# Kernel optimization log

Measured on AMD Instinct MI355X. Metric: run time of the kernel, lower is better.

Reference implementation:

```python
import jax, jax.numpy as jnp
import numpy as np

N = 8192
FEAT = 200
SEG = FEAT // 4  # 50
OUT = 300


def setup_inputs() -> dict:
    key = jax.random.key(0)
    ks = jax.random.split(key, 10)
    x = jax.random.normal(ks[0], (N, FEAT), dtype=jnp.float32)
    # row-normalized-ish dense adjacencies so activations stay O(1)
    A_S = jax.random.uniform(ks[1], (N, N), dtype=jnp.float32) / N
    A_F = jax.random.uniform(ks[2], (N, N), dtype=jnp.float32) / N
    gcn_W = jax.random.normal(ks[3], (SEG, SEG), dtype=jnp.float32) / np.sqrt(SEG)
    gcn_b = jnp.zeros((SEG,), dtype=jnp.float32)
    # 12 forget gates: order s1,s2,s3,f1,f2,f3,s1b,s2b,s3b,f1b,f2b,f3b
    gates_W = jax.random.normal(ks[4], (12, 2 * SEG, SEG), dtype=jnp.float32)
    gates_b = jax.random.normal(ks[5], (12, SEG), dtype=jnp.float32)
    proj_W = jax.random.normal(ks[6], (8 * SEG, OUT), dtype=jnp.float32) / np.sqrt(8 * SEG)
    proj_b = jnp.zeros((OUT,), dtype=jnp.float32)
    return {"x": x, "A_S": A_S, "A_F": A_F, "gcn_W": gcn_W, "gcn_b": gcn_b,
            "gates_W": gates_W, "gates_b": gates_b, "proj_W": proj_W, "proj_b": proj_b}


def _lgfm(x, A_S, A_F, gcn_W, gcn_b, gates_W, gates_b, proj_W, proj_b):
    seg = x.shape[1] // 4

    def gcn(h, A):
        # Kipf GraphConvolution: relu(A @ (h @ W) + b); dropout inactive (eval)
        return jax.nn.relu(A @ (h @ gcn_W) + gcn_b)

    def gate(i, h1, h2):
        a = jax.nn.sigmoid(jnp.concatenate([h1, h2], axis=1) @ gates_W[i] + gates_b[i])
        return a * h1

    GS1, GS2, GS3, GF1, GF2, GF3 = 0, 1, 2, 3, 4, 5
    GS1B, GS2B, GS3B, GF1B, GF2B, GF3B = 6, 7, 8, 9, 10, 11

    x1, x2, x3, x4 = x[:, :seg], x[:, seg:2 * seg], x[:, 2 * seg:3 * seg], x[:, 3 * seg:]

    # forward branch (F path then S gating)
    t1_XF1 = x1 + gcn(x1, A_F)
    t1_XS1 = gcn(x1, A_S)
    t1_XF2 = 0.2 * t1_XS1 + 0.8 * gcn(t1_XF1, A_F)
    t2_XF1 = x2 + gcn(x2, A_F)
    t2_XS1 = gcn(x2, A_S)
    t2_XS1 = t2_XS1 + gate(GS1, t1_XS1, t2_XS1)
    t2_XF2 = 0.2 * t2_XS1 + 0.8 * gcn(t2_XF1, A_F)
    t2_XF2 = gate(GF1, t1_XF2, t2_XF2) + t2_XF2
    t3_XF1 = 0.2 * x3 + 0.8 * gcn(x3, A_F)
    t3_XS1 = gcn(x3, A_S)
    t3_XS1 = t3_XS1 + gate(GS2, t2_XS1, t3_XS1)
    t3_XF2 = 0.2 * t3_XS1 + 0.8 * gcn(t3_XF1, A_F)
    t3_XF2 = gate(GF2, t2_XF2, t3_XF2) + t3_XF2
    t4_XF1 = x4 + gcn(x4, A_F)
    t4_XS1 = gcn(x4, A_S)
    t4_XS1 = t4_XS1 + gate(GS3, t3_XS1, t4_XS1)
    t4_XF2 = 0.2 * t4_XS1 + 0.8 * gcn(t4_XF1, A_F)
    t4_XF2 = gate(GF3, t3_XF2, t4_XF2) + t4_XF2

    # mirrored branch (S path then F gating)
    t1_XS1b = x1 + gcn(x1, A_S)
    t1_XF1b = gcn(x1, A_F)
    t1_XS2 = 0.2 * t1_XF1b + 0.8 * gcn(t1_XS1b, A_S)
    t2_XS1b = x2 + gcn(x2, A_S)
    t2_XF1b = gcn(x2, A_F)
    t2_XF1b = t2_XF1b + gate(GF1B, t1_XF1b, t2_XF1b)
    t2_XS2 = 0.2 * t2_XF1b + 0.8 * gcn(t2_XS1b, A_S)
    t2_XS2 = gate(GS1B, t1_XS2, t2_XS2) + t2_XS2
    t3_XS1b = 0.2 * x3 + 0.8 * gcn(x3, A_S)
    t3_XF1b = gcn(x3, A_F)
    t3_XF1b = t3_XF1b + gate(GF2B, t2_XF1b, t3_XF1b)
    t3_XS2 = 0.2 * t3_XF1b + 0.8 * gcn(t3_XS1b, A_S)
    t3_XS2 = gate(GS2B, t2_XS2, t3_XS2) + t3_XS2
    t4_XS1b = x4 + gcn(x4, A_S)
    t4_XF1b = gcn(x4, A_F)
    t4_XF1b = t4_XF1b + gate(GF3B, t3_XF1b, t4_XF1b)
    t4_XS2 = 0.2 * t4_XF1b + 0.8 * gcn(t4_XS1b, A_S)
    t4_XS2 = gate(GS3B, t3_XS2, t4_XS2) + t4_XS2

    h_L = jnp.concatenate([t1_XF2, t1_XS2, t2_XF2, t2_XS2,
                           t3_XF2, t3_XS2, t4_XF2, t4_XS2], axis=1)
    return h_L @ proj_W + proj_b


def reference(x, A_S, A_F, gcn_W, gcn_b, gates_W, gates_b, proj_W, proj_b):
    return _lgfm(x, A_S, A_F, gcn_W, gcn_b, gates_W, gates_b, proj_W, proj_b)
```

## Files before the change

kernel.cpp:

```cpp
#include <hip/hip_runtime.h>
#include <math.h>

typedef float float4v __attribute__((ext_vector_type(4)));
typedef __attribute__((ext_vector_type(4))) float f32x4;
typedef __attribute__((ext_vector_type(8))) short short8v;
typedef __attribute__((ext_vector_type(8))) unsigned short ushort8v;

#define NROW 8192
#define FEAT 200
#define OUTC 300
#define ZLD  256
#define HLK  448
#define HLN  384

__device__ __forceinline__ unsigned short f2bf(float x) {
  unsigned u = __float_as_uint(x);
  return (unsigned short)((u + 0x7fffu + ((u >> 16) & 1u)) >> 16);
}

__global__ __launch_bounds__(256) void zmul_t_kernel(
    const float* __restrict__ x, const float* __restrict__ W,
    unsigned short* __restrict__ Zt) {
  __shared__ float Ws[2500];
  __shared__ float hs[16][200];
  __shared__ float zbuf[16][256];
  int t = threadIdx.x;
  int r0 = blockIdx.x * 16;
  for (int i = t; i < 2500; i += 256) Ws[i] = W[i];
  for (int i = t; i < 16 * FEAT; i += 256)
    hs[0][i] = x[(size_t)r0 * FEAT + i];
  __syncthreads();
  for (int i = t; i < 16 * 256; i += 256) {
    int row = i >> 8, j = i & 255;
    float acc = 0.f;
    if (j < FEAT) {
      int s = j / 50, jj = j % 50;
      const float* hrow = &hs[row][s * 50];
      #pragma unroll 5
      for (int k = 0; k < 50; ++k) acc += hrow[k] * Ws[k * 50 + jj];
    }
    zbuf[row][j] = acc;
  }
  __syncthreads();
  unsigned int* Ztu = (unsigned int*)Zt;
  for (int i = t; i < 256 * 8; i += 256) {
    int j = i >> 3, w2 = i & 7;
    unsigned int lo = f2bf(zbuf[2 * w2][j]);
    unsigned int hi = f2bf(zbuf[2 * w2 + 1][j]);
    Ztu[((j * NROW + r0) >> 1) + w2] = lo | (hi << 16);
  }
}

__global__ __launch_bounds__(512, 4) void gemm_cvt_spill_kernel(
    const float* __restrict__ AF, const float* __restrict__ AS,
    const unsigned short* __restrict__ ZtF,
    const unsigned short* __restrict__ ZtS,
    float* __restrict__ Cpart,
    unsigned short* __restrict__ AbF_o, unsigned short* __restrict__ AbS_o) {
  int d = blockIdx.x;
  int L = (d & 7) * 64 + (d >> 3);
  int cb  = L & 1;
  int mat = (L >> 1) & 1;
  int ks  = (L >> 2) & 1;
  int rb  = L >> 3;

  const float* __restrict__ A = mat ? AS : AF;
  const unsigned short* __restrict__ Zt = mat ? ZtS : ZtF;
  unsigned short* __restrict__ Abo = mat ? AbS_o : AbF_o;

  int t = threadIdx.x;
  int lane = t & 63, wv = t >> 6;
  int row0 = rb * 128, n0 = cb * 128, k0 = ks * 4096;

  __shared__ short As[2][128 * 64];
  __shared__ short Bs[2][128 * 64];

  int srcAf[2], dstA[2];
  #pragma unroll
  for (int i = 0; i < 2; ++i) {
    int cc = i * 512 + t;
    int m = cc >> 3, s = cc & 7;
    srcAf[i] = (row0 + m) * NROW + s * 8;
    dstA[i] = m * 64 + ((s ^ (m & 7)) * 8);
  }
  int srcB[2], ldsDstB[2];
  #pragma unroll
  for (int i = 0; i < 2; ++i) {
    int c = i * 512 + t;
    int m = c >> 3, sl = c & 7;
    srcB[i] = (n0 + m) * NROW + ((sl ^ (m & 7)) * 8);
    ldsDstB[i] = (i * 512 + wv * 64) * 8;
  }

  f32x4 aA0[2], aA1[2], aB0[2], aB1[2];

#define STAGE_B(buf, kt)                                                              \
  {                                                                                   \
    _Pragma("unroll")                                                                 \
    for (int i = 0; i < 2; ++i)                                                       \
      __builtin_amdgcn_global_load_lds(                                               \
          (const __attribute__((address_space(1))) void*)(Zt + srcB[i] + (kt)),       \
          (__attribute__((address_space(3))) void*)(&Bs[buf][ldsDstB[i]]), 16, 0, 0); \
  }
#define LOAD_BANK(b0, b1, kt)                              \
  {                                                        \
    _Pragma("unroll")                                      \
    for (int i = 0; i < 2; ++i) {                          \
      b0[i] = *(const f32x4*)&A[srcAf[i] + (kt)];          \
      b1[i] = *(const f32x4*)&A[srcAf[i] + (kt) + 4];      \
    }                                                      \
  }
#define WRITE_BANK(buf, b0, b1, kt, spill)                                              \
  {                                                                                     \
    _Pragma("unroll")                                                                   \
    for (int i = 0; i < 2; ++i) {                                                       \
      unsigned u0_, u1_, u2_, u3_;                                                      \
      asm("v_cvt_pk_bf16_f32 %0, %1, %2" : "=v"(u0_) : "v"(b0[i][0]), "v"(b0[i][1]));   \
      asm("v_cvt_pk_bf16_f32 %0, %1, %2" : "=v"(u1_) : "v"(b0[i][2]), "v"(b0[i][3]));   \
      asm("v_cvt_pk_bf16_f32 %0, %1, %2" : "=v"(u2_) : "v"(b1[i][0]), "v"(b1[i][1]));   \
      asm("v_cvt_pk_bf16_f32 %0, %1, %2" : "=v"(u3_) : "v"(b1[i][2]), "v"(b1[i][3]));   \
      union { unsigned u[4]; short8v v; } pk_;                                          \
      pk_.u[0] = u0_; pk_.u[1] = u1_; pk_.u[2] = u2_; pk_.u[3] = u3_;                   \
      *(short8v*)&As[buf][dstA[i]] = pk_.v;                                             \
      if (spill) *(short8v*)&Abo[(size_t)srcAf[i] + (kt)] = pk_.v;                      \
    }                                                                                   \
  }
#define MFMA_TILE(buf)                                                                  \
  {                                                                                     \
    _Pragma("unroll")                                                                   \
    for (int kk = 0; kk < 2; ++kk) {                                                    \
      int slot = kk * 4 + l4;                                                           \
      short8v a[2], b[4];                                                               \
      _Pragma("unroll")                                                                 \
      for (int i = 0; i < 2; ++i) {                                                     \
        int m = m0 + i * 16 + l15;                                                      \
        a[i] = *(const short8v*)&As[buf][m * 64 + ((slot ^ (m & 7)) * 8)];              \
      }                                                                                 \
      _Pragma("unroll")                                                                 \
      for (int j = 0; j < 4; ++j) {                                                     \
        int n = n0w + j * 16 + l15;                                                     \
        b[j] = *(const short8v*)&Bs[buf][n * 64 + ((slot ^ (n & 7)) * 8)];              \
      }                                                                                 \
      _Pragma("unroll")                                                                 \
      for (int i = 0; i < 2; ++i)                                                       \
        _Pragma("unroll")                                                               \
        for (int j = 0; j < 4; ++j)                                                     \
          acc[i][j] = __builtin_amdgcn_mfma_f32_16x16x32_bf16(a[i], b[j], acc[i][j], 0, 0, 0); \
  } }

  f32x4 acc[2][4];
  #pragma unroll
  for (int i = 0; i < 2; ++i)
    #pragma unroll
    for (int j = 0; j < 4; ++j) acc[i][j] = (f32x4)0.f;

  int m0 = (wv >> 1) * 32, n0w = (wv & 1) * 64;
  int l15 = lane & 15, l4 = lane >> 4;

  LOAD_BANK(aA0, aA1, k0)
  LOAD_BANK(aB0, aB1, k0 + 64)
  STAGE_B(0, k0)
  WRITE_BANK(0, aA0, aA1, k0, (cb == 0))
  __syncthreads();

  for (int itp = 0; itp < 32; ++itp) {
    {
      int it = 2 * itp;
      if (it + 1 < 64) STAGE_B(1, k0 + (it + 1) * 64)
      if (it + 2 < 64) LOAD_BANK(aA0, aA1, k0 + (it + 2) * 64)
      MFMA_TILE(0)
      if (it + 1 < 64) {
        bool sp = (cb == ((it + 1) >= 32 ? 1 : 0));
        WRITE_BANK(1, aB0, aB1, k0 + (it + 1) * 64, sp)
      }
      __syncthreads();
    }
    {
      int it = 2 * itp + 1;
      if (it + 1 < 64) STAGE_B(0, k0 + (it + 1) * 64)
      if (it + 2 < 64) LOAD_BANK(aB0, aB1, k0 + (it + 2) * 64)
      MFMA_TILE(1)
      if (it + 1 < 64) {
        bool sp = (cb == ((it + 1) >= 32 ? 1 : 0));
        WRITE_BANK(0, aA0, aA1, k0 + (it + 1) * 64, sp)
      }
      __syncthreads();
    }
  }
#undef STAGE_B
#undef LOAD_BANK
#undef WRITE_BANK
#undef MFMA_TILE

  int s = mat * 2 + ks;
  #pragma unroll
  for (int i = 0; i < 2; ++i) {
    #pragma unroll
    for (int j = 0; j < 4; ++j) {
      int c = n0 + n0w + j * 16 + l15;
      #pragma unroll
      for (int q = 0; q < 4; ++q) {
        int r = row0 + m0 + i * 16 + l4 * 4 + q;
        Cpart[((size_t)(s * NROW + r) << 8) + c] = acc[i][j][q];
      }
    }
  }
}

__global__ __launch_bounds__(512, 4) void gemm_pair_kernel(
    const unsigned short* __restrict__ AbF,
    const unsigned short* __restrict__ AbS,
    const unsigned short* __restrict__ ZtF,
    const unsigned short* __restrict__ ZtS,
    float* __restrict__ Cpart) {
  int d = blockIdx.x;
  int L = (d & 7) * 64 + (d >> 3);
  int cb  = L & 1;
  int mat = (L >> 1) & 1;
  int ks  = (L >> 2) & 1;
  int rb  = L >> 3;

  const unsigned short* __restrict__ Ab = mat ? AbS : AbF;
  const unsigned short* __restrict__ Zt = mat ? ZtS : ZtF;

  int t = threadIdx.x;
  int lane = t & 63, wv = t >> 6;
  int row0 = rb * 128, n0 = cb * 128, k0 = ks * 4096;

  __shared__ short As[2][128 * 64];
  __shared__ short Bs[2][128 * 64];

  int srcA[2], srcB[2], ldsDst[2];
  #pragma unroll
  for (int i = 0; i < 2; ++i) {
    int c = i * 512 + t;
    int m = c >> 3, sl = c & 7;
    int sw = ((sl ^ (m & 7)) * 8);
    srcA[i] = (row0 + m) * NROW + sw;
    srcB[i] = (n0 + m) * NROW + sw;
    ldsDst[i] = (i * 512 + wv * 64) * 8;
  }

#define STAGE_TILE(buf, kt)                                                          \
  {                                                                                  \
    _Pragma("unroll")                                                                \
    for (int i = 0; i < 2; ++i) {                                                    \
      __builtin_amdgcn_global_load_lds(                                              \
          (const __attribute__((address_space(1))) void*)(Ab + srcA[i] + (kt)),      \
          (__attribute__((address_space(3))) void*)(&As[buf][ldsDst[i]]), 16, 0, 0); \
      __builtin_amdgcn_global_load_lds(                                              \
          (const __attribute__((address_space(1))) void*)(Zt + srcB[i] + (kt)),      \
          (__attribute__((address_space(3))) void*)(&Bs[buf][ldsDst[i]]), 16, 0, 0); \
    }                                                                                \
  }

  f32x4 acc[2][4];
  #pragma unroll
  for (int i = 0; i < 2; ++i)
    #pragma unroll
    for (int j = 0; j < 4; ++j) acc[i][j] = (f32x4)0.f;

  int m0 = (wv >> 1) * 32, n0w = (wv & 1) * 64;
  int l15 = lane & 15, l4 = lane >> 4;

  int cur = 0;
  STAGE_TILE(0, k0)
  __syncthreads();

  for (int it = 0; it < 64; ++it) {
    if (it + 1 < 64) STAGE_TILE(cur ^ 1, k0 + (it + 1) * 64)

    #pragma unroll
    for (int kk = 0; kk < 2; ++kk) {
      int slot = kk * 4 + l4;
      short8v a[2], b[4];
      #pragma unroll
      for (int i = 0; i < 2; ++i) {
        int m = m0 + i * 16 + l15;
        a[i] = *(const short8v*)&As[cur][m * 64 + ((slot ^ (m & 7)) * 8)];
      }
      #pragma unroll
      for (int j = 0; j < 4; ++j) {
        int n = n0w + j * 16 + l15;
        b[j] = *(const short8v*)&Bs[cur][n * 64 + ((slot ^ (n & 7)) * 8)];
      }
      #pragma unroll
      for (int i = 0; i < 2; ++i)
        #pragma unroll
        for (int j = 0; j < 4; ++j)
          acc[i][j] = __builtin_amdgcn_mfma_f32_16x16x32_bf16(a[i], b[j], acc[i][j], 0, 0, 0);
    }
    __syncthreads();
    cur ^= 1;
  }
#undef STAGE_TILE

  int s = mat * 2 + ks;
  #pragma unroll
  for (int i = 0; i < 2; ++i) {
    #pragma unroll
    for (int j = 0; j < 4; ++j) {
      int c = n0 + n0w + j * 16 + l15;
      #pragma unroll
      for (int q = 0; q < 4; ++q) {
        int r = row0 + m0 + i * 16 + l4 * 4 + q;
        Cpart[((size_t)(s * NROW + r) << 8) + c] = acc[i][j][q];
      }
    }
  }
}

__global__ __launch_bounds__(256) void reduce_zmul_kernel(
    const float* __restrict__ Cpart, const float* __restrict__ bias,
    const float* __restrict__ x, const float* __restrict__ W,
    float* __restrict__ GF0, float* __restrict__ GS0,
    unsigned short* __restrict__ ZtF, unsigned short* __restrict__ ZtS) {
  __shared__ float Ws[2500];
  __shared__ float hs[16][200];
  __shared__ float zbuf[16][256];
  int t = threadIdx.x;
  int r0 = blockIdx.x * 16;
  int w = t >> 6, j = t & 63;
  bool act = j < 50;
  int rbase = r0 + w * 4;
  for (int i = t; i < 2500; i += 256) Ws[i] = W[i];

  const float alpha[4] = {1.f, 1.f, 0.2f, 1.f};
  const float beta[4]  = {1.f, 1.f, 0.8f, 1.f};
  float gf[4][4], gs[4][4];
  if (act) {
    float bv = bias[j];
    #pragma unroll
    for (int r = 0; r < 4; ++r)
      #pragma unroll
      for (int s = 0; s < 4; ++s) {
        int c = s * 50 + j;
        size_t base = (((size_t)(rbase + r)) << 8) + c;
        float vF = Cpart[base] + Cpart[base + (size_t)NROW * 256];
        float vS = Cpart[base + (size_t)2 * NROW * 256] + Cpart[base + (size_t)3 * NROW * 256];
        gf[r][s] = fmaxf(vF + bv, 0.f);
        gs[r][s] = fmaxf(vS + bv, 0.f);
        GF0[(size_t)(rbase + r) * FEAT + c] = gf[r][s];
        GS0[(size_t)(rbase + r) * FEAT + c] = gs[r][s];
      }
    #pragma unroll
    for (int r = 0; r < 4; ++r)
      #pragma unroll
      for (int s = 0; s < 4; ++s)
        hs[w * 4 + r][s * 50 + j] =
            alpha[s] * x[(size_t)(rbase + r) * FEAT + s * 50 + j] + beta[s] * gf[r][s];
  }
  __syncthreads();
  for (int i = t; i < 16 * 256; i += 256) {
    int row = i >> 8, jj = i & 255;
    float acc = 0.f;
    if (jj < FEAT) {
      int s = jj / 50, j2 = jj % 50;
      const float* hrow = &hs[row][s * 50];
      #pragma unroll 5
      for (int k = 0; k < 50; ++k) acc += hrow[k] * Ws[k * 50 + j2];
    }
    zbuf[row][jj] = acc;
  }
  __syncthreads();
  {
    unsigned int* Ztu = (unsigned int*)ZtF;
    for (int i = t; i < 256 * 8; i += 256) {
      int j2 = i >> 3, w2 = i & 7;
      unsigned int lo = f2bf(zbuf[2 * w2][j2]);
      unsigned int hi = f2bf(zbuf[2 * w2 + 1][j2]);
      Ztu[((j2 * NROW + r0) >> 1) + w2] = lo | (hi << 16);
    }
  }
  if (act) {
    #pragma unroll
    for (int r = 0; r < 4; ++r)
      #pragma unroll
      for (int s = 0; s < 4; ++s)
        hs[w * 4 + r][s * 50 + j] =
            alpha[s] * x[(size_t)(rbase + r) * FEAT + s * 50 + j] + beta[s] * gs[r][s];
  }
  __syncthreads();
  for (int i = t; i < 16 * 256; i += 256) {
    int row = i >> 8, jj = i & 255;
    float acc = 0.f;
    if (jj < FEAT) {
      int s = jj / 50, j2 = jj % 50;
      const float* hrow = &hs[row][s * 50];
      #pragma unroll 5
      for (int k = 0; k < 50; ++k) acc += hrow[k] * Ws[k * 50 + j2];
    }
    zbuf[row][jj] = acc;
  }
  __syncthreads();
  {
    unsigned int* Ztu = (unsigned int*)ZtS;
    for (int i = t; i < 256 * 8; i += 256) {
      int j2 = i >> 3, w2 = i & 7;
      unsigned int lo = f2bf(zbuf[2 * w2][j2]);
      unsigned int hi = f2bf(zbuf[2 * w2 + 1][j2]);
      Ztu[((j2 * NROW + r0) >> 1) + w2] = lo | (hi << 16);
    }
  }
}

__device__ __forceinline__ void gate4(const float* __restrict__ gWi, const float* __restrict__ gbi,
                                      float* hsw, float* Wg, int t, int j, bool act,
                                      const float* h1, const float* h2, float* aout) {
  if (act) {
    #pragma unroll
    for (int r = 0; r < 4; ++r) { hsw[r * 128 + j] = h1[r]; hsw[r * 128 + 64 + j] = h2[r]; }
  }
  {
    const float4v* src = (const float4v*)gWi;
    float4v* dst = (float4v*)Wg;
    #pragma unroll
    for (int u = 0; u < 5; ++u) {
      int i = t + 256 * u;
      if (i < 1250) dst[i] = src[i];
    }
  }
  __syncthreads();
  float acc0 = 0.f, acc1 = 0.f, acc2 = 0.f, acc3 = 0.f;
  if (act) {
    float bv = gbi[j];
    acc0 = bv; acc1 = bv; acc2 = bv; acc3 = bv;
    #pragma unroll 2
    for (int k = 0; k < 50; ++k) {
      float wv = Wg[k * 50 + j];
      acc0 += hsw[0 * 128 + k] * wv;
      acc1 += hsw[1 * 128 + k] * wv;
      acc2 += hsw[2 * 128 + k] * wv;
      acc3 += hsw[3 * 128 + k] * wv;
    }
    #pragma unroll 2
    for (int k = 0; k < 50; ++k) {
      float wv = Wg[(50 + k) * 50 + j];
      acc0 += hsw[0 * 128 + 64 + k] * wv;
      acc1 += hsw[1 * 128 + 64 + k] * wv;
      acc2 += hsw[2 * 128 + 64 + k] * wv;
      acc3 += hsw[3 * 128 + 64 + k] * wv;
    }
  }
  __syncthreads();
  float accs[4] = {acc0, acc1, acc2, acc3};
  #pragma unroll
  for (int r = 0; r < 4; ++r) {
    float a = 1.f / (1.f + expf(-accs[r]));
    aout[r] = a * h1[r];
  }
}

__global__ __launch_bounds__(256) void reduce_chain_kernel(
    const float* __restrict__ Cpart, const float* __restrict__ bias,
    const float* __restrict__ GF0, const float* __restrict__ GS0,
    const float* __restrict__ gW, const float* __restrict__ gb,
    unsigned short* __restrict__ hLb) {
  __shared__ float hsb[4 * 512];
  __shared__ float Wg[5000];
  int t = threadIdx.x;
  int w = t >> 6, j = t & 63;
  bool act = j < 50;
  float* hsw = &hsb[w * 512];
  int rbase = blockIdx.x * 16 + w * 4;

  float gf0[4][4], gs0[4][4], gf1[4][4], gs1[4][4];
  if (act) {
    float bv = bias[j];
    #pragma unroll
    for (int r = 0; r < 4; ++r)
      #pragma unroll
      for (int s = 0; s < 4; ++s) {
        int c = s * 50 + j;
        size_t base = (((size_t)(rbase + r)) << 8) + c;
        float vF = Cpart[base] + Cpart[base + (size_t)NROW * 256];
        float vS = Cpart[base + (size_t)2 * NROW * 256] + Cpart[base + (size_t)3 * NROW * 256];
        gf1[r][s] = fmaxf(vF + bv, 0.f);
        gs1[r][s] = fmaxf(vS + bv, 0.f);
        gf0[r][s] = GF0[(size_t)(rbase + r) * FEAT + c];
        gs0[r][s] = GS0[(size_t)(rbase + r) * FEAT + c];
      }
  }
  if (!act) {
    for (int p = j - 50; p < 48; p += 14)
      #pragma unroll
      for (int r = 0; r < 4; ++r)
        hLb[(size_t)(rbase + r) * HLK + 400 + p] = 0;
  }

  float xf2[4], xs1[4], pre[4], a[4], h1t[4], h2t[4];
  #pragma unroll
  for (int r = 0; r < 4; ++r) xf2[r] = 0.2f * gs0[r][0] + 0.8f * gf1[r][0];
  if (act) {
    #pragma unroll
    for (int r = 0; r < 4; ++r) hLb[(size_t)(rbase + r) * HLK + 0 + j] = f2bf(xf2[r]);
  }
  #pragma unroll
  for (int r = 0; r < 4; ++r) { h1t[r] = gs0[r][0]; h2t[r] = gs0[r][1]; }
  gate4(gW + 0 * 5000, gb + 0 * 50, hsw, Wg, t, j, act, h1t, h2t, a);
  #pragma unroll
  for (int r = 0; r < 4; ++r) xs1[r] = gs0[r][1] + a[r];
  #pragma unroll
  for (int r = 0; r < 4; ++r) pre[r] = 0.2f * xs1[r] + 0.8f * gf1[r][1];
  gate4(gW + 3 * 5000, gb + 3 * 50, hsw, Wg, t, j, act, xf2, pre, a);
  #pragma unroll
  for (int r = 0; r < 4; ++r) xf2[r] = a[r] + pre[r];
  if (act) {
    #pragma unroll
    for (int r = 0; r < 4; ++r) hLb[(size_t)(rbase + r) * HLK + 100 + j] = f2bf(xf2[r]);
  }
  #pragma unroll
  for (int r = 0; r < 4; ++r) { h1t[r] = xs1[r]; h2t[r] = gs0[r][2]; }
  gate4(gW + 1 * 5000, gb + 1 * 50, hsw, Wg, t, j, act, h1t, h2t, a);
  #pragma unroll
  for (int r = 0; r < 4; ++r) xs1[r] = gs0[r][2] + a[r];
  #pragma unroll
  for (int r = 0; r < 4; ++r) pre[r] = 0.2f * xs1[r] + 0.8f * gf1[r][2];
  gate4(gW + 4 * 5000, gb + 4 * 50, hsw, Wg, t, j, act, xf2, pre, a);
  #pragma unroll
  for (int r = 0; r < 4; ++r) xf2[r] = a[r] + pre[r];
  if (act) {
    #pragma unroll
    for (int r = 0; r < 4; ++r) hLb[(size_t)(rbase + r) * HLK + 200 + j] = f2bf(xf2[r]);
  }
  #pragma unroll
  for (int r = 0; r < 4; ++r) { h1t[r] = xs1[r]; h2t[r] = gs0[r][3]; }
  gate4(gW + 2 * 5000, gb + 2 * 50, hsw, Wg, t, j, act, h1t, h2t, a);
  #pragma unroll
  for (int r = 0; r < 4; ++r) xs1[r] = gs0[r][3] + a[r];
  #pragma unroll
  for (int r = 0; r < 4; ++r) pre[r] = 0.2f * xs1[r] + 0.8f * gf1[r][3];
  gate4(gW + 5 * 5000, gb + 5 * 50, hsw, Wg, t, j, act, xf2, pre, a);
  #pragma unroll
  for (int r = 0; r < 4; ++r) xf2[r] = a[r] + pre[r];
  if (act) {
    #pragma unroll
    for (int r = 0; r < 4; ++r) hLb[(size_t)(rbase + r) * HLK + 300 + j] = f2bf(xf2[r]);
  }

  float xs2[4], xf1b[4];
  #pragma unroll
  for (int r = 0; r < 4; ++r) xs2[r] = 0.2f * gf0[r][0] + 0.8f * gs1[r][0];
  if (act) {
    #pragma unroll
    for (int r = 0; r < 4; ++r) hLb[(size_t)(rbase + r) * HLK + 50 + j] = f2bf(xs2[r]);
  }
  #pragma unroll
  for (int r = 0; r < 4; ++r) { h1t[r] = gf0[r][0]; h2t[r] = gf0[r][1]; }
  gate4(gW + 9 * 5000, gb + 9 * 50, hsw, Wg, t, j, act, h1t, h2t, a);
  #pragma unroll
  for (int r = 0; r < 4; ++r) xf1b[r] = gf0[r][1] + a[r];
  #pragma unroll
  for (int r = 0; r < 4; ++r) pre[r] = 0.2f * xf1b[r] + 0.8f * gs1[r][1];
  gate4(gW + 6 * 5000, gb + 6 * 50, hsw, Wg, t, j, act, xs2, pre, a);
  #pragma unroll
  for (int r = 0; r < 4; ++r) xs2[r] = a[r] + pre[r];
  if (act) {
    #pragma unroll
    for (int r = 0; r < 4; ++r) hLb[(size_t)(rbase + r) * HLK + 150 + j] = f2bf(xs2[r]);
  }
  #pragma unroll
  for (int r = 0; r < 4; ++r) { h1t[r] = xf1b[r]; h2t[r] = gf0[r][2]; }
  gate4(gW + 10 * 5000, gb + 10 * 50, hsw, Wg, t, j, act, h1t, h2t, a);
  #pragma unroll
  for (int r = 0; r < 4; ++r) xf1b[r] = gf0[r][2] + a[r];
  #pragma unroll
  for (int r = 0; r < 4; ++r) pre[r] = 0.2f * xf1b[r] + 0.8f * gs1[r][2];
  gate4(gW + 7 * 5000, gb + 7 * 50, hsw, Wg, t, j, act, xs2, pre, a);
  #pragma unroll
  for (int r = 0; r < 4; ++r) xs2[r] = a[r] + pre[r];
  if (act) {
    #pragma unroll
    for (int r = 0; r < 4; ++r) hLb[(size_t)(rbase + r) * HLK + 250 + j] = f2bf(xs2[r]);
  }
  #pragma unroll
  for (int r = 0; r < 4; ++r) { h1t[r] = xf1b[r]; h2t[r] = gf0[r][3]; }
  gate4(gW + 11 * 5000, gb + 11 * 50, hsw, Wg, t, j, act, h1t, h2t, a);
  #pragma unroll
  for (int r = 0; r < 4; ++r) xf1b[r] = gf0[r][3] + a[r];
  #pragma unroll
  for (int r = 0; r < 4; ++r) pre[r] = 0.2f * xf1b[r] + 0.8f * gs1[r][3];
  gate4(gW + 8 * 5000, gb + 8 * 50, hsw, Wg, t, j, act, xs2, pre, a);
  #pragma unroll
  for (int r = 0; r < 4; ++r) xs2[r] = a[r] + pre[r];
  if (act) {
    #pragma unroll
    for (int r = 0; r < 4; ++r) hLb[(size_t)(rbase + r) * HLK + 350 + j] = f2bf(xs2[r]);
  }
}

__global__ __launch_bounds__(256) void wconv_kernel(
    const float* __restrict__ pW, unsigned short* __restrict__ Wtb) {
  int i = blockIdx.x * 256 + threadIdx.x;
  if (i >= HLN * HLK) return;
  int n = i / HLK, k = i % HLK;
  float v = (n < OUTC && k < 400) ? pW[k * OUTC + n] : 0.f;
  Wtb[i] = f2bf(v);
}

__global__ __launch_bounds__(256, 2) void proj_gemm_kernel(
    const unsigned short* __restrict__ hLb,
    const unsigned short* __restrict__ Wtb,
    const float* __restrict__ pb, float* __restrict__ outp) {
  int d = blockIdx.x;
  int L = (d & 7) * 24 + (d >> 3);
  int rb = L / 3, cb = L % 3;

  int t = threadIdx.x;
  int lane = t & 63, wv = t >> 6;
  int row0 = rb * 128, n0 = cb * 128;

  __shared__ short As[2][128 * 64];
  __shared__ short Bs[2][128 * 64];

  int srcA[4], srcB[4], ldsDst[4];
  #pragma unroll
  for (int i = 0; i < 4; ++i) {
    int c = i * 256 + t;
    int m = c >> 3, sl = c & 7;
    int sw = ((sl ^ (m & 7)) * 8);
    srcA[i] = (row0 + m) * HLK + sw;
    srcB[i] = (n0 + m) * HLK + sw;
    ldsDst[i] = (i * 256 + wv * 64) * 8;
  }

#define STAGE_TILE(buf, kt)                                                          \
  {                                                                                  \
    _Pragma("unroll")                                                                \
    for (int i = 0; i < 4; ++i) {                                                    \
      __builtin_amdgcn_global_load_lds(                                              \
          (const __attribute__((address_space(1))) void*)(hLb + srcA[i] + (kt)),     \
          (__attribute__((address_space(3))) void*)(&As[buf][ldsDst[i]]), 16, 0, 0); \
      __builtin_amdgcn_global_load_lds(                                              \
          (const __attribute__((address_space(1))) void*)(Wtb + srcB[i] + (kt)),     \
          (__attribute__((address_space(3))) void*)(&Bs[buf][ldsDst[i]]), 16, 0, 0); \
    }                                                                                \
  }

  f32x4 acc[4][4];
  #pragma unroll
  for (int i = 0; i < 4; ++i)
    #pragma unroll
    for (int j = 0; j < 4; ++j) acc[i][j] = (f32x4)0.f;

  int m0 = (wv >> 1) * 64, n0w = (wv & 1) * 64;
  int l15 = lane & 15, l4 = lane >> 4;

  int cur = 0;
  STAGE_TILE(0, 0)
  __syncthreads();

  for (int it = 0; it < 7; ++it) {
    if (it + 1 < 7) STAGE_TILE(cur ^ 1, (it + 1) * 64)

    #pragma unroll
    for (int kk = 0; kk < 2; ++kk) {
      int slot = kk * 4 + l4;
      short8v a[4], b[4];
      #pragma unroll
      for (int i = 0; i < 4; ++i) {
        int m = m0 + i * 16 + l15;
        a[i] = *(const short8v*)&As[cur][m * 64 + ((slot ^ (m & 7)) * 8)];
        int n = n0w + i * 16 + l15;
        b[i] = *(const short8v*)&Bs[cur][n * 64 + ((slot ^ (n & 7)) * 8)];
      }
      #pragma unroll
      for (int i = 0; i < 4; ++i)
        #pragma unroll
        for (int j = 0; j < 4; ++j)
          acc[i][j] = __builtin_amdgcn_mfma_f32_16x16x32_bf16(a[i], b[j], acc[i][j], 0, 0, 0);
    }
    __syncthreads();
    cur ^= 1;
  }
#undef STAGE_TILE

  #pragma unroll
  for (int i = 0; i < 4; ++i) {
    #pragma unroll
    for (int j = 0; j < 4; ++j) {
      int c = n0 + n0w + j * 16 + l15;
      if (c < OUTC) {
        float b = pb[c];
        #pragma unroll
        for (int q = 0; q < 4; ++q) {
          int r = row0 + m0 + i * 16 + l4 * 4 + q;
          outp[(size_t)r * OUTC + c] = acc[i][j][q] + b;
        }
      }
    }
  }
}

__global__ __launch_bounds__(256) void zmul_f32_kernel(
    const float* __restrict__ x, const float* __restrict__ g,
    const float* __restrict__ W,
    float a0, float a1, float a2, float a3,
    float b0, float b1, float b2, float b3,
    float* __restrict__ Zp) {
  __shared__ float Ws[2500];
  __shared__ float hs[200];
  int t = threadIdx.x;
  for (int i = t; i < 2500; i += 256) Ws[i] = W[i];
  float alpha[4] = {a0, a1, a2, a3};
  float beta[4]  = {b0, b1, b2, b3};
  int s  = (t < 200) ? (t / 50) : 0;
  int jj = (t < 200) ? (t % 50) : 0;
  int r0 = blockIdx.x * 32;
  for (int rr = 0; rr < 32; ++rr) {
    int row = r0 + rr;
    __syncthreads();
    if (t < 200) hs[t] = alpha[s] * x[row * FEAT + t] + beta[s] * g[row * FEAT + t];
    __syncthreads();
    float acc = 0.f;
    if (t < 200) {
      const float* hrow = &hs[s * 50];
      #pragma unroll 5
      for (int k = 0; k < 50; ++k) acc += hrow[k] * Ws[k * 50 + jj];
    }
    Zp[row * ZLD + t] = (t < 200) ? acc : 0.f;
  }
}

#define BM 64
#define BN 64
#define BK 32
#define ALD 68
__global__ __launch_bounds__(256) void gemm_relu_kernel(
    const float* __restrict__ A, const float* __restrict__ Zp,
    const float* __restrict__ bias, float* __restrict__ C) {
  int wg  = blockIdx.x;
  int swz = (wg & 7) * 64 + (wg >> 3);
  int rb  = swz >> 2;
  int cb  = swz & 3;
  int t   = threadIdx.x;
  int rt  = t >> 4, ct = t & 15;
  __shared__ __align__(16) float As[BK][ALD];
  __shared__ __align__(16) float Zs[BK][BN];
  float acc[4][4];
  #pragma unroll
  for (int i = 0; i < 4; ++i)
    #pragma unroll
    for (int j = 0; j < 4; ++j) acc[i][j] = 0.f;
  const int row0 = rb * BM, col0 = cb * BN;
  int ar = t >> 3;
  int ak = (t & 7) * 4;
  int zr = t >> 4;
  int zc = (t & 15) * 4;
  const float4v* A4 = (const float4v*)A;
  const float4v* Z4 = (const float4v*)Zp;
  float4v a0, a1, z0, z1;
  a0 = A4[((size_t)(row0 + ar) * NROW + 0 + ak) >> 2];
  a1 = A4[((size_t)(row0 + ar + 32) * NROW + 0 + ak) >> 2];
  z0 = Z4[((0 + zr) * ZLD + col0 + zc) >> 2];
  z1 = Z4[((0 + zr + 16) * ZLD + col0 + zc) >> 2];
  for (int kt = 0; kt < NROW; kt += BK) {
    __syncthreads();
    #pragma unroll
    for (int u = 0; u < 4; ++u) As[ak + u][ar] = a0[u];
    #pragma unroll
    for (int u = 0; u < 4; ++u) As[ak + u][ar + 32] = a1[u];
    *(float4v*)&Zs[zr][zc]      = z0;
    *(float4v*)&Zs[zr + 16][zc] = z1;
    __syncthreads();
    int kn = kt + BK;
    if (kn < NROW) {
      a0 = A4[((size_t)(row0 + ar) * NROW + kn + ak) >> 2];
      a1 = A4[((size_t)(row0 + ar + 32) * NROW + kn + ak) >> 2];
      z0 = Z4[((kn + zr) * ZLD + col0 + zc) >> 2];
      z1 = Z4[((kn + zr + 16) * ZLD + col0 + zc) >> 2];
    }
    #pragma unroll
    for (int k = 0; k < BK; ++k) {
      float4v av = *(const float4v*)&As[k][rt * 4];
      float4v zv = *(const float4v*)&Zs[k][ct * 4];
      #pragma unroll
      for (int i = 0; i < 4; ++i)
        #pragma unroll
        for (int j = 0; j < 4; ++j) acc[i][j] += av[i] * zv[j];
    }
  }
  #pragma unroll
  for (int i = 0; i < 4; ++i) {
    int grow = row0 + rt * 4 + i;
    #pragma unroll
    for (int j = 0; j < 4; ++j) {
      int gcol = col0 + ct * 4 + j;
      if (gcol < FEAT) {
        float v = acc[i][j] + bias[gcol % 50];
        C[(size_t)grow * FEAT + gcol] = fmaxf(v, 0.f);
      }
    }
  }
}

__global__ __launch_bounds__(256) void chain_top_kernel(
    const float* __restrict__ GS0, const float* __restrict__ GF1,
    const float* __restrict__ gW, const float* __restrict__ gb,
    unsigned short* __restrict__ hLb) {
  __shared__ float hsb[4 * 512];
  __shared__ float Wg[5000];
  int t = threadIdx.x;
  int w = t >> 6, j = t & 63;
  bool act = j < 50;
  float* hsw = &hsb[w * 512];
  int rbase = blockIdx.x * 16 + w * 4;
  float gs[4][4], gf[4][4];
  #pragma unroll
  for (int r = 0; r < 4; ++r)
    #pragma unroll
    for (int s = 0; s < 4; ++s) { gs[r][s] = 0.f; gf[r][s] = 0.f; }
  if (act) {
    #pragma unroll
    for (int r = 0; r < 4; ++r)
      #pragma unroll
      for (int s = 0; s < 4; ++s) {
        gs[r][s] = GS0[(size_t)(rbase + r) * FEAT + s * 50 + j];
        gf[r][s] = GF1[(size_t)(rbase + r) * FEAT + s * 50 + j];
      }
  }
  float xf2[4], xs1[4], pre[4], a[4], h1t[4], h2t[4];
  #pragma unroll
  for (int r = 0; r < 4; ++r) xf2[r] = 0.2f * gs[r][0] + 0.8f * gf[r][0];
  if (act) {
    #pragma unroll
    for (int r = 0; r < 4; ++r) hLb[(size_t)(rbase + r) * HLK + 0 + j] = f2bf(xf2[r]);
  }
  #pragma unroll
  for (int r = 0; r < 4; ++r) { h1t[r] = gs[r][0]; h2t[r] = gs[r][1]; }
  gate4(gW + 0 * 5000, gb + 0 * 50, hsw, Wg, t, j, act, h1t, h2t, a);
  #pragma unroll
  for (int r = 0; r < 4; ++r) xs1[r] = gs[r][1] + a[r];
  #pragma unroll
  for (int r = 0; r < 4; ++r) pre[r] = 0.2f * xs1[r] + 0.8f * gf[r][1];
  gate4(gW + 3 * 5000, gb + 3 * 50, hsw, Wg, t, j, act, xf2, pre, a);
  #pragma unroll
  for (int r = 0; r < 4; ++r) xf2[r] = a[r] + pre[r];
  if (act) {
    #pragma unroll
    for (int r = 0; r < 4; ++r) hLb[(size_t)(rbase + r) * HLK + 100 + j] = f2bf(xf2[r]);
  }
  #pragma unroll
  for (int r = 0; r < 4; ++r) { h1t[r] = xs1[r]; h2t[r] = gs[r][2]; }
  gate4(gW + 1 * 5000, gb + 1 * 50, hsw, Wg, t, j, act, h1t, h2t, a);
  #pragma unroll
  for (int r = 0; r < 4; ++r) xs1[r] = gs[r][2] + a[r];
  #pragma unroll
  for (int r = 0; r < 4; ++r) pre[r] = 0.2f * xs1[r] + 0.8f * gf[r][2];
  gate4(gW + 4 * 5000, gb + 4 * 50, hsw, Wg, t, j, act, xf2, pre, a);
  #pragma unroll
  for (int r = 0; r < 4; ++r) xf2[r] = a[r] + pre[r];
  if (act) {
    #pragma unroll
    for (int r = 0; r < 4; ++r) hLb[(size_t)(rbase + r) * HLK + 200 + j] = f2bf(xf2[r]);
  }
  #pragma unroll
  for (int r = 0; r < 4; ++r) { h1t[r] = xs1[r]; h2t[r] = gs[r][3]; }
  gate4(gW + 2 * 5000, gb + 2 * 50, hsw, Wg, t, j, act, h1t, h2t, a);
  #pragma unroll
  for (int r = 0; r < 4; ++r) xs1[r] = gs[r][3] + a[r];
  #pragma unroll
  for (int r = 0; r < 4; ++r) pre[r] = 0.2f * xs1[r] + 0.8f * gf[r][3];
  gate4(gW + 5 * 5000, gb + 5 * 50, hsw, Wg, t, j, act, xf2, pre, a);
  #pragma unroll
  for (int r = 0; r < 4; ++r) xf2[r] = a[r] + pre[r];
  if (act) {
    #pragma unroll
    for (int r = 0; r < 4; ++r) hLb[(size_t)(rbase + r) * HLK + 300 + j] = f2bf(xf2[r]);
  }
}

__global__ __launch_bounds__(256) void chain_bottom_kernel(
    const float* __restrict__ GF0, const float* __restrict__ GS1,
    const float* __restrict__ gW, const float* __restrict__ gb,
    unsigned short* __restrict__ hLb) {
  __shared__ float hsb[4 * 512];
  __shared__ float Wg[5000];
  int t = threadIdx.x;
  int w = t >> 6, j = t & 63;
  bool act = j < 50;
  float* hsw = &hsb[w * 512];
  int rbase = blockIdx.x * 16 + w * 4;
  float gf0[4][4], gs1[4][4];
  #pragma unroll
  for (int r = 0; r < 4; ++r)
    #pragma unroll
    for (int s = 0; s < 4; ++s) { gf0[r][s] = 0.f; gs1[r][s] = 0.f; }
  if (act) {
    #pragma unroll
    for (int r = 0; r < 4; ++r)
      #pragma unroll
      for (int s = 0; s < 4; ++s) {
        gf0[r][s] = GF0[(size_t)(rbase + r) * FEAT + s * 50 + j];
        gs1[r][s] = GS1[(size_t)(rbase + r) * FEAT + s * 50 + j];
      }
  }
  float xs2[4], xf1b[4], pre[4], a[4], h1t[4], h2t[4];
  #pragma unroll
  for (int r = 0; r < 4; ++r) xs2[r] = 0.2f * gf0[r][0] + 0.8f * gs1[r][0];
  if (act) {
    #pragma unroll
    for (int r = 0; r < 4; ++r) hLb[(size_t)(rbase + r) * HLK + 50 + j] = f2bf(xs2[r]);
  }
  #pragma unroll
  for (int r = 0; r < 4; ++r) { h1t[r] = gf0[r][0]; h2t[r] = gf0[r][1]; }
  gate4(gW + 9 * 5000, gb + 9 * 50, hsw, Wg, t, j, act, h1t, h2t, a);
  #pragma unroll
  for (int r = 0; r < 4; ++r) xf1b[r] = gf0[r][1] + a[r];
  #pragma unroll
  for (int r = 0; r < 4; ++r) pre[r] = 0.2f * xf1b[r] + 0.8f * gs1[r][1];
  gate4(gW + 6 * 5000, gb + 6 * 50, hsw, Wg, t, j, act, xs2, pre, a);
  #pragma unroll
  for (int r = 0; r < 4; ++r) xs2[r] = a[r] + pre[r];
  if (act) {
    #pragma unroll
    for (int r = 0; r < 4; ++r) hLb[(size_t)(rbase + r) * HLK + 150 + j] = f2bf(xs2[r]);
  }
  #pragma unroll
  for (int r = 0; r < 4; ++r) { h1t[r] = xf1b[r]; h2t[r] = gf0[r][2]; }
  gate4(gW + 10 * 5000, gb + 10 * 50, hsw, Wg, t, j, act, h1t, h2t, a);
  #pragma unroll
  for (int r = 0; r < 4; ++r) xf1b[r] = gf0[r][2] + a[r];
  #pragma unroll
  for (int r = 0; r < 4; ++r) pre[r] = 0.2f * xf1b[r] + 0.8f * gs1[r][2];
  gate4(gW + 7 * 5000, gb + 7 * 50, hsw, Wg, t, j, act, xs2, pre, a);
  #pragma unroll
  for (int r = 0; r < 4; ++r) xs2[r] = a[r] + pre[r];
  if (act) {
    #pragma unroll
    for (int r = 0; r < 4; ++r) hLb[(size_t)(rbase + r) * HLK + 250 + j] = f2bf(xs2[r]);
  }
  #pragma unroll
  for (int r = 0; r < 4; ++r) { h1t[r] = xf1b[r]; h2t[r] = gf0[r][3]; }
  gate4(gW + 11 * 5000, gb + 11 * 50, hsw, Wg, t, j, act, h1t, h2t, a);
  #pragma unroll
  for (int r = 0; r < 4; ++r) xf1b[r] = gf0[r][3] + a[r];
  #pragma unroll
  for (int r = 0; r < 4; ++r) pre[r] = 0.2f * xf1b[r] + 0.8f * gs1[r][3];
  gate4(gW + 8 * 5000, gb + 8 * 50, hsw, Wg, t, j, act, xs2, pre, a);
  #pragma unroll
  for (int r = 0; r < 4; ++r) xs2[r] = a[r] + pre[r];
  if (act) {
    #pragma unroll
    for (int r = 0; r < 4; ++r) hLb[(size_t)(rbase + r) * HLK + 350 + j] = f2bf(xs2[r]);
  }
}

extern "C" void kernel_launch(void* const* d_in, const int* in_sizes, int n_in,
                              void* d_out, int out_size, void* d_ws, size_t ws_size,
                              hipStream_t stream) {
  const float* x       = (const float*)d_in[0];
  const float* A_S     = (const float*)d_in[1];
  const float* A_F     = (const float*)d_in[2];
  const float* gcn_W   = (const float*)d_in[3];
  const float* gcn_b   = (const float*)d_in[4];
  const float* gates_W = (const float*)d_in[5];
  const float* gates_b = (const float*)d_in[6];
  const float* proj_W  = (const float*)d_in[7];
  const float* proj_b  = (const float*)d_in[8];
  float* out = (float*)d_out;

  const size_t szAb    = (size_t)NROW * NROW * 2;
  const size_t szZt    = (size_t)256 * NROW * 2;
  const size_t szCpart = (size_t)4 * NROW * 256 * 4;
  const size_t szG     = (size_t)NROW * FEAT * 4;
  const size_t szHLb   = (size_t)NROW * HLK * 2;
  const size_t szWtb   = (size_t)HLN * HLK * 2;
  const size_t need = 2 * szAb + 3 * szZt + szCpart + 2 * szG + szHLb + szWtb;

  if (ws_size >= need) {
    char* w = (char*)d_ws;
    unsigned short* AbF  = (unsigned short*)w;           w += szAb;
    unsigned short* AbS  = (unsigned short*)w;           w += szAb;
    unsigned short* Zt0  = (unsigned short*)w;           w += szZt;
    unsigned short* Zt1F = (unsigned short*)w;           w += szZt;
    unsigned short* Zt1S = (unsigned short*)w;           w += szZt;
    float* Cpart = (float*)w;                            w += szCpart;
    float* GF0 = (float*)w;                              w += szG;
    float* GS0 = (float*)w;                              w += szG;
    unsigned short* hLb = (unsigned short*)w;            w += szHLb;
    unsigned short* Wtb = (unsigned short*)w;

    wconv_kernel<<<(HLN * HLK + 255) / 256, 256, 0, stream>>>(proj_W, Wtb);
    zmul_t_kernel<<<512, 256, 0, stream>>>(x, gcn_W, Zt0);

    gemm_cvt_spill_kernel<<<512, 512, 0, stream>>>(A_F, A_S, Zt0, Zt0, Cpart, AbF, AbS);
    reduce_zmul_kernel<<<512, 256, 0, stream>>>(Cpart, gcn_b, x, gcn_W, GF0, GS0, Zt1F, Zt1S);

    gemm_pair_kernel<<<512, 512, 0, stream>>>(AbF, AbS, Zt1F, Zt1S, Cpart);
    reduce_chain_kernel<<<512, 256, 0, stream>>>(Cpart, gcn_b, GF0, GS0, gates_W, gates_b, hLb);

    proj_gemm_kernel<<<192, 256, 0, stream>>>(hLb, Wtb, proj_b, out);
  } else {
    char* w = (char*)d_ws;
    float* Z   = (float*)w;                              w += (size_t)NROW * ZLD * 4;
    float* GF0 = (float*)w;                              w += szG;
    float* GS0 = (float*)w;                              w += szG;
    float* GF1 = (float*)w;                              w += szG;
    float* GS1 = (float*)w;                              w += szG;
    unsigned short* hLb = (unsigned short*)w;            w += szHLb;
    unsigned short* Wtb = (unsigned short*)w;

    hipMemsetAsync(hLb, 0, szHLb, stream);
    wconv_kernel<<<(HLN * HLK + 255) / 256, 256, 0, stream>>>(proj_W, Wtb);

    zmul_f32_kernel<<<256, 256, 0, stream>>>(x, x, gcn_W, 1.f, 1.f, 1.f, 1.f, 0.f, 0.f, 0.f, 0.f, Z);
    gemm_relu_kernel<<<512, 256, 0, stream>>>(A_F, Z, gcn_b, GF0);
    gemm_relu_kernel<<<512, 256, 0, stream>>>(A_S, Z, gcn_b, GS0);
    zmul_f32_kernel<<<256, 256, 0, stream>>>(x, GF0, gcn_W, 1.f, 1.f, 0.2f, 1.f, 1.f, 1.f, 0.8f, 1.f, Z);
    gemm_relu_kernel<<<512, 256, 0, stream>>>(A_F, Z, gcn_b, GF1);
    zmul_f32_kernel<<<256, 256, 0, stream>>>(x, GS0, gcn_W, 1.f, 1.f, 0.2f, 1.f, 1.f, 1.f, 0.8f, 1.f, Z);
    gemm_relu_kernel<<<512, 256, 0, stream>>>(A_S, Z, gcn_b, GS1);

    chain_top_kernel<<<512, 256, 0, stream>>>(GS0, GF1, gates_W, gates_b, hLb);
    chain_bottom_kernel<<<512, 256, 0, stream>>>(GF0, GS1, gates_W, gates_b, hLb);
    proj_gemm_kernel<<<192, 256, 0, stream>>>(hLb, Wtb, proj_b, out);
  }
}
```

Baseline: 498.3 us.

## Triple-buffer B tiles with async LDS loads and lighter barriers in GEMM

The fp32-to-bf16 converting GEMM now triple-buffers the B (Zt) LDS tiles and issues the async global-to-LDS load two iterations ahead instead of one. Full __syncthreads is replaced by a barrier that waits only on lgkmcnt, so outstanding vmem loads can stay in flight across the barrier. The block-index decode is also permuted in both GEMM kernels so that neighbouring blocks differ by matrix and k-split rather than column block, which changes L2 sharing of the A rows. The extra B buffer raises LDS use, which may reduce occupancy, and relying on lgkmcnt alone for the global_load_lds data is a correctness risk.

```diff
diff --git a/kernel.cpp b/kernel.cpp
--- a/kernel.cpp
+++ b/kernel.cpp
@@ -17,6 +17,13 @@
   unsigned u = __float_as_uint(x);
   return (unsigned short)((u + 0x7fffu + ((u >> 16) & 1u)) >> 16);
 }
+
+#define BARSYNC()                                              \
+  {                                                            \
+    asm volatile("s_waitcnt lgkmcnt(0)" ::: "memory");         \
+    __builtin_amdgcn_s_barrier();                              \
+    __builtin_amdgcn_sched_barrier(0);                         \
+  }
 
 __global__ __launch_bounds__(256) void zmul_t_kernel(
     const float* __restrict__ x, const float* __restrict__ W,
@@ -59,9 +66,9 @@
     unsigned short* __restrict__ AbF_o, unsigned short* __restrict__ AbS_o) {
   int d = blockIdx.x;
   int L = (d & 7) * 64 + (d >> 3);
-  int cb  = L & 1;
-  int mat = (L >> 1) & 1;
-  int ks  = (L >> 2) & 1;
+  int mat = L & 1;
+  int ks  = (L >> 1) & 1;
+  int cb  = (L >> 2) & 1;
   int rb  = L >> 3;
 
   const float* __restrict__ A = mat ? AS : AF;
@@ -73,7 +80,7 @@
   int row0 = rb * 128, n0 = cb * 128, k0 = ks * 4096;
 
   __shared__ short As[2][128 * 64];
-  __shared__ short Bs[2][128 * 64];
+  __shared__ short Bs[3][128 * 64];
 
   int srcAf[2], dstA[2];
   #pragma unroll
@@ -110,7 +117,7 @@
       b1[i] = *(const f32x4*)&A[srcAf[i] + (kt) + 4];      \
     }                                                      \
   }
-#define WRITE_BANK(buf, b0, b1, kt, spill)                                              \
+#define WRITE_BANK(abuf, b0, b1, kt, spill)                                             \
   {                                                                                     \
     _Pragma("unroll")                                                                   \
     for (int i = 0; i < 2; ++i) {                                                       \
@@ -121,11 +128,11 @@
       asm("v_cvt_pk_bf16_f32 %0, %1, %2" : "=v"(u3_) : "v"(b1[i][2]), "v"(b1[i][3]));   \
       union { unsigned u[4]; short8v v; } pk_;                                          \
       pk_.u[0] = u0_; pk_.u[1] = u1_; pk_.u[2] = u2_; pk_.u[3] = u3_;                   \
-      *(short8v*)&As[buf][dstA[i]] = pk_.v;                                             \
+      *(short8v*)&As[abuf][dstA[i]] = pk_.v;                                            \
       if (spill) *(short8v*)&Abo[(size_t)srcAf[i] + (kt)] = pk_.v;                      \
     }                                                                                   \
   }
-#define MFMA_TILE(buf)                                                                  \
+#define MFMA_TILE(abuf, bbuf)                                                           \
   {                                                                                     \
     _Pragma("unroll")                                                                   \
     for (int kk = 0; kk < 2; ++kk) {                                                    \
@@ -134,12 +141,12 @@
       _Pragma("unroll")                                                                 \
       for (int i = 0; i < 2; ++i) {                                                     \
         int m = m0 + i * 16 + l15;                                                      \
-        a[i] = *(const short8v*)&As[buf][m * 64 + ((slot ^ (m & 7)) * 8)];              \
+        a[i] = *(const short8v*)&As[abuf][m * 64 + ((slot ^ (m & 7)) * 8)];             \
       }                                                                                 \
       _Pragma("unroll")                                                                 \
       for (int j = 0; j < 4; ++j) {                                                     \
         int n = n0w + j * 16 + l15;                                                     \
-        b[j] = *(const short8v*)&Bs[buf][n * 64 + ((slot ^ (n & 7)) * 8)];              \
+        b[j] = *(const short8v*)&Bs[bbuf][n * 64 + ((slot ^ (n & 7)) * 8)];             \
       }                                                                                 \
       _Pragma("unroll")                                                                 \
       for (int i = 0; i < 2; ++i)                                                       \
@@ -157,34 +164,39 @@
   int m0 = (wv >> 1) * 32, n0w = (wv & 1) * 64;
   int l15 = lane & 15, l4 = lane >> 4;
 
+  STAGE_B(0, k0)
+  STAGE_B(1, k0 + 64)
   LOAD_BANK(aA0, aA1, k0)
   LOAD_BANK(aB0, aB1, k0 + 64)
-  STAGE_B(0, k0)
   WRITE_BANK(0, aA0, aA1, k0, (cb == 0))
-  __syncthreads();
+  BARSYNC()
 
   for (int itp = 0; itp < 32; ++itp) {
     {
       int it = 2 * itp;
-      if (it + 1 < 64) STAGE_B(1, k0 + (it + 1) * 64)
-      if (it + 2 < 64) LOAD_BANK(aA0, aA1, k0 + (it + 2) * 64)
-      MFMA_TILE(0)
+      if (it + 2 < 64) {
+        STAGE_B((it + 2) % 3, k0 + (it + 2) * 64)
+        LOAD_BANK(aA0, aA1, k0 + (it + 2) * 64)
+      }
+      MFMA_TILE(0, (it % 3))
       if (it + 1 < 64) {
         bool sp = (cb == ((it + 1) >= 32 ? 1 : 0));
         WRITE_BANK(1, aB0, aB1, k0 + (it + 1) * 64, sp)
       }
-      __syncthreads();
+      BARSYNC()
     }
     {
       int it = 2 * itp + 1;
-      if (it + 1 < 64) STAGE_B(0, k0 + (it + 1) * 64)
-      if (it + 2 < 64) LOAD_BANK(aB0, aB1, k0 + (it + 2) * 64)
-      MFMA_TILE(1)
+      if (it + 2 < 64) {
+        STAGE_B((it + 2) % 3, k0 + (it + 2) * 64)
+        LOAD_BANK(aB0, aB1, k0 + (it + 2) * 64)
+      }
+      MFMA_TILE(1, (it % 3))
       if (it + 1 < 64) {
         bool sp = (cb == ((it + 1) >= 32 ? 1 : 0));
         WRITE_BANK(0, aA0, aA1, k0 + (it + 1) * 64, sp)
       }
-      __syncthreads();
+      BARSYNC()
     }
   }
 #undef STAGE_B
@@ -215,9 +227,9 @@
     float* __restrict__ Cpart) {
   int d = blockIdx.x;
   int L = (d & 7) * 64 + (d >> 3);
-  int cb  = L & 1;
-  int mat = (L >> 1) & 1;
-  int ks  = (L >> 2) & 1;
+  int mat = L & 1;
+  int ks  = (L >> 1) & 1;
+  int cb  = (L >> 2) & 1;
   int rb  = L >> 3;
 
   const unsigned short* __restrict__ Ab = mat ? AbS : AbF;
```

Result: no change. 493.2 us (-1.0%).
